# Optimization experiments

Hardware: AMD Instinct MI355X
Metric: run time of the kernel (lower is better)

## Reference

```python
import jax, jax.numpy as jnp
import numpy as np

B, N, H, D = 1, 4096, 16, 64
C = H * D  # 1024
SCALE = D ** -0.5


def setup_inputs() -> dict:
    key = jax.random.key(0)
    k1, k2, k3, k4 = jax.random.split(key, 4)
    x = jax.random.normal(k1, (B, N, C), dtype=jnp.float32)
    # torch nn.Linear weights: [out_features, in_features]; y = x @ W.T + b
    w_qkv = jax.random.normal(k2, (3 * C, C), dtype=jnp.float32) * 0.02
    w_proj = jax.random.normal(k3, (C, C), dtype=jnp.float32) * 0.02
    b_proj = jax.random.normal(k4, (C,), dtype=jnp.float32) * 0.02
    return {"x": x, "w_qkv": w_qkv, "w_proj": w_proj, "b_proj": b_proj}


def reference(x, w_qkv, w_proj, b_proj):
    Bn, Nn, Cn = x.shape
    # fused QKV projection (no bias)
    qkv = jnp.einsum('bnc,oc->bno', x, w_qkv)            # [B,N,3C]
    qkv = qkv.reshape(Bn, Nn, 3, H, D)
    q = jnp.transpose(qkv[:, :, 0], (0, 2, 1, 3))        # [B,H,N,D]
    k = jnp.transpose(qkv[:, :, 1], (0, 2, 1, 3))
    v = jnp.transpose(qkv[:, :, 2], (0, 2, 1, 3))
    attn = jnp.einsum('bhnd,bhmd->bhnm', q, k) * SCALE   # [B,H,N,N]
    causal_mask = jnp.triu(jnp.ones((Nn, Nn), dtype=bool), k=1)
    attn = jnp.where(causal_mask, -jnp.inf, attn)
    attn = jax.nn.softmax(attn, axis=-1)
    out = jnp.einsum('bhnm,bhmd->bhnd', attn, v)          # [B,H,N,D]
    out = jnp.transpose(out, (0, 2, 1, 3)).reshape(Bn, Nn, Cn)
    out = jnp.einsum('bnc,oc->bno', out, w_proj) + b_proj
    return out
```

## Files before the change

### kernel.cpp

```cpp
#include <hip/hip_runtime.h>
#include <hip/hip_bf16.h>
#include <stdint.h>
#include <stddef.h>

using bf16 = __hip_bfloat16;
typedef short short8 __attribute__((ext_vector_type(8)));
typedef short short4v __attribute__((ext_vector_type(4)));
typedef short short2v __attribute__((ext_vector_type(2)));
typedef float f32x4 __attribute__((ext_vector_type(4)));

#define MFMA16(A, B, C) __builtin_amdgcn_mfma_f32_16x16x32_bf16(A, B, C, 0, 0, 0)
#define MFMA16K16(A, B, C) __builtin_amdgcn_mfma_f32_16x16x16bf16_1k(A, B, C, 0, 0, 0)
#define GLOAD_LDS(g, l) __builtin_amdgcn_global_load_lds( \
    (const __attribute__((address_space(1))) void*)(g),   \
    (__attribute__((address_space(3))) void*)(l), 16, 0, 0)

constexpr int AN  = 4096;
constexpr int NH  = 16;
constexpr int HD  = 64;
constexpr int CC  = 1024;
constexpr int C3  = 3072;
constexpr float QSCALE = 0.125f * 1.4426950408889634f;

__device__ inline short bf16s(float f) {
    bf16 h = __float2bfloat16(f);
    return *reinterpret_cast<short*>(&h);
}
__device__ inline float bf2f(short s) {
    return __uint_as_float(((unsigned)(unsigned short)s) << 16);
}
__device__ inline short4v pack4(float a, float b, float c, float d) {
    union { short4v s4; __hip_bfloat162 h2[2]; } u;
    u.h2[0] = __float22bfloat162_rn(make_float2(a, b));
    u.h2[1] = __float22bfloat162_rn(make_float2(c, d));
    return u.s4;
}

__global__ void detect_mode(const unsigned short* __restrict__ xraw,
                            int* __restrict__ mode) {
    const int lane = threadIdx.x;
    int crazy = 0;
    #pragma unroll
    for (int i = 0; i < 4; ++i) {
        const unsigned short u = xraw[lane * 4 + i];
        const int e = (u >> 7) & 0xFF;
        if (e >= 134 || (e != 0 && e <= 110)) ++crazy;
    }
    #pragma unroll
    for (int off = 32; off > 0; off >>= 1)
        crazy += __shfl_down(crazy, off, 64);
    if (lane == 0) *mode = (crazy >= 8) ? 1 : 0;
}

__global__ void cast_in(const void* __restrict__ src, bf16* __restrict__ dst,
                        int n, const int* __restrict__ mode) {
    const int i = (blockIdx.x * blockDim.x + threadIdx.x) * 8;
    if (i >= n) return;
    if (*mode) {
        const float* s = (const float*)src;
        float4 a = *(const float4*)(s + i);
        float4 b = *(const float4*)(s + i + 4);
        short8 o;
        o[0] = bf16s(a.x); o[1] = bf16s(a.y); o[2] = bf16s(a.z); o[3] = bf16s(a.w);
        o[4] = bf16s(b.x); o[5] = bf16s(b.y); o[6] = bf16s(b.z); o[7] = bf16s(b.w);
        *(short8*)(dst + i) = o;
    } else {
        *(short8*)(dst + i) = *(const short8*)((const short*)src + i);
    }
}

__global__ void cast_bias(const void* __restrict__ src, float* __restrict__ dst,
                          int n, const int* __restrict__ mode) {
    const int i = blockIdx.x * blockDim.x + threadIdx.x;
    if (i >= n) return;
    dst[i] = (*mode) ? ((const float*)src)[i]
                     : __bfloat162float(((const bf16*)src)[i]);
}

constexpr int BM = 128, BN = 128, BK = 32;

template<int MODE>
__global__ __launch_bounds__(256, 2) void gemm_bt(
    const bf16* __restrict__ A, const bf16* __restrict__ Bw,
    const float* __restrict__ bias, void* __restrict__ Cout,
    bf16* __restrict__ vTout, const int* __restrict__ mode,
    int M, int K, int O)
{
    __shared__ bf16 As[BM * BK];
    __shared__ bf16 Bs[BN * BK];

    const int tid  = threadIdx.x;
    const int wave = tid >> 6;
    const int lane = tid & 63;
    const int quad = lane >> 4;
    const int l16  = lane & 15;
    const int wr   = wave >> 1;
    const int wc   = wave & 1;
    const int m0   = blockIdx.y * BM;
    const int o0   = blockIdx.x * BN;

    const int srow = lane >> 2;
    const int scol = (lane & 3) * 8;

    f32x4 acc[4][4] = {};

    for (int k0 = 0; k0 < K; k0 += BK) {
        __syncthreads();
        #pragma unroll
        for (int c = 0; c < 2; ++c) {
            const int rbase = wave * 32 + c * 16;
            GLOAD_LDS(A + (size_t)(m0 + rbase + srow) * K + k0 + scol, &As[rbase * BK]);
            GLOAD_LDS(Bw + (size_t)(o0 + rbase + srow) * K + k0 + scol, &Bs[rbase * BK]);
        }
        __syncthreads();

        short8 af[4], bfr[4];
        #pragma unroll
        for (int i = 0; i < 4; ++i)
            af[i] = *(const short8*)&As[(wr * 64 + i * 16 + l16) * BK + quad * 8];
        #pragma unroll
        for (int j = 0; j < 4; ++j)
            bfr[j] = *(const short8*)&Bs[(wc * 64 + j * 16 + l16) * BK + quad * 8];
        #pragma unroll
        for (int i = 0; i < 4; ++i)
            #pragma unroll
            for (int j = 0; j < 4; ++j)
                acc[i][j] = MFMA16(af[i], bfr[j], acc[i][j]);
    }

    if (MODE == 1 && o0 >= 2 * CC) {
        #pragma unroll
        for (int j = 0; j < 4; ++j) {
            const int vc = o0 - 2 * CC + wc * 64 + j * 16 + l16;
            #pragma unroll
            for (int i = 0; i < 4; ++i) {
                const int row0 = m0 + wr * 64 + i * 16 + quad * 4;
                *(short4v*)&vTout[(size_t)vc * AN + row0] =
                    pack4(acc[i][j][0], acc[i][j][1], acc[i][j][2], acc[i][j][3]);
            }
        }
        return;
    }
    const float qs = (MODE == 1 && o0 < CC) ? QSCALE : 1.0f;
    const bool f32out = (MODE == 2) && (*mode != 0);
    #pragma unroll
    for (int j = 0; j < 4; ++j) {
        const int col = o0 + wc * 64 + j * 16 + l16;
        const float bv = bias ? bias[col] : 0.0f;
        #pragma unroll
        for (int i = 0; i < 4; ++i) {
            const int row = m0 + wr * 64 + i * 16 + quad * 4;
            #pragma unroll
            for (int r = 0; r < 4; ++r) {
                const float v = acc[i][j][r] * qs + bv;
                const size_t idx = (size_t)(row + r) * O + col;
                if (f32out) ((float*)Cout)[idx] = v;
                else        ((bf16*)Cout)[idx]  = __float2bfloat16(v);
            }
        }
    }
}

constexpr int TK = 64;

__global__ __launch_bounds__(256, 4) void attn5(
    const bf16* __restrict__ qkv, const bf16* __restrict__ vT,
    bf16* __restrict__ pOn, float* __restrict__ pl)
{
    __shared__ bf16 Ks[2][TK * HD];
    __shared__ bf16 Vs[2][HD * TK];

    const int tid  = threadIdx.x;
    const int wave = tid >> 6;
    const int lane = tid & 63;
    const int quad = lane >> 4;
    const int l16  = lane & 15;
    const int h7   = l16 & 7;
    const int h    = blockIdx.x & 15;
    const int t    = blockIdx.x >> 4;

    short4v ones;
    ones[0] = (short)0x3F80; ones[1] = (short)0x3F80;
    ones[2] = (short)0x3F80; ones[3] = (short)0x3F80;

    const int sr = lane >> 3;
    const int pc = lane & 7;

    #pragma unroll 1
    for (int pp = 0; pp < 2; ++pp) {
        const int tile = pp ? 63 - t : t;
        const int nIt  = tile + 1;
        const int i0   = pp ? ((64 - t) + 1) >> 1 : 0;
        const int i1   = pp ? 64 - t : (t + 2) >> 1;
        const int half = pp;
        const int qw   = tile * 64 + wave * 16;

        short8 qf0, qf1;
        {
            const bf16* qp = qkv + (size_t)(qw + l16) * C3 + h * HD + quad * 8;
            qf0 = *(const short8*)qp;
            qf1 = *(const short8*)(qp + 32);
        }

        f32x4 acc_l = {};
        f32x4 acc_o[4] = {};

        if (i0 < i1) {
            const bf16 *kp[2], *vp[2];
            #pragma unroll
            for (int c = 0; c < 2; ++c) {
                const int row = wave * 16 + c * 8 + sr;
                const int lc  = pc ^ (row & 7);
                kp[c] = qkv + (size_t)(i0 * TK + row) * C3 + CC + h * HD + lc * 8;
                vp[c] = vT + (size_t)(h * HD + row) * AN + i0 * TK + lc * 8;
            }
            auto stage = [&](int p) {
                #pragma unroll
                for (int c = 0; c < 2; ++c) {
                    const int rb = wave * 16 + c * 8;
                    GLOAD_LDS(kp[c], &Ks[p][rb * HD]);
                    GLOAD_LDS(vp[c], &Vs[p][rb * TK]);
                    kp[c] += (size_t)TK * C3;
                    vp[c] += TK;
                }
            };
            stage(0);
            __syncthreads();
            const bool hasdiag = (i1 == nIt);

            for (int it = i0; it < i1; ++it) {
                const int p = (it - i0) & 1;
                if (it + 1 < i1) stage(p ^ 1);

                f32x4 st[4];
                #pragma unroll
                for (int tt = 0; tt < 4; ++tt) {
                    const int row = tt * 16 + l16;
                    short8 kf0 = *(const short8*)&Ks[p][row * HD + ((quad ^ h7) * 8)];
                    short8 kf1 = *(const short8*)&Ks[p][row * HD + (((quad + 4) ^ h7) * 8)];
                    f32x4 a = {};
                    a = MFMA16(kf0, qf0, a);
                    a = MFMA16(kf1, qf1, a);
                    st[tt] = a;
                }

                if (hasdiag && it == i1 - 1) {
                    const int q = qw + l16;
                    const int kv0 = it * TK;
                    #pragma unroll
                    for (int tt = 0; tt < 4; ++tt)
                        #pragma unroll
                        for (int r = 0; r < 4; ++r) {
                            const int kv = kv0 + tt * 16 + quad * 4 + r;
                            st[tt][r] = (kv <= q) ? exp2f(st[tt][r]) : 0.0f;
                        }
                } else {
                    #pragma unroll
                    for (int tt = 0; tt < 4; ++tt)
                        #pragma unroll
                        for (int r = 0; r < 4; ++r)
                            st[tt][r] = exp2f(st[tt][r]);
                }

                #pragma unroll
                for (int tt = 0; tt < 4; ++tt) {
                    const short4v bp = pack4(st[tt][0], st[tt][1], st[tt][2], st[tt][3]);
                    acc_l = MFMA16K16(ones, bp, acc_l);
                    const int pc2 = (2 * tt + (quad >> 1)) ^ h7;
                    #pragma unroll
                    for (int dt = 0; dt < 4; ++dt) {
                        const int row = dt * 16 + l16;
                        short4v vf = *(const short4v*)&Vs[p][row * TK + pc2 * 8 + (quad & 1) * 4];
                        acc_o[dt] = MFMA16K16(vf, bp, acc_o[dt]);
                    }
                }
                __syncthreads();
            }
        }

        const size_t base = (size_t)half * AN * CC + (size_t)(qw + l16) * CC + h * HD;
        #pragma unroll
        for (int dt = 0; dt < 4; ++dt) {
            const int d0 = dt * 16 + quad * 4;
            *(short4v*)&pOn[base + d0] =
                pack4(acc_o[dt][0], acc_o[dt][1], acc_o[dt][2], acc_o[dt][3]);
        }
        if (quad == 0)
            pl[(size_t)half * NH * AN + (size_t)h * AN + qw + l16] = acc_l[0];
    }
}

__global__ __launch_bounds__(128) void combine_halves(
    const bf16* __restrict__ pOn, const float* __restrict__ pl,
    bf16* __restrict__ outp)
{
    const int q  = blockIdx.x;
    const int c0 = threadIdx.x * 8;
    const int h  = c0 >> 6;
    const float l0 = pl[(size_t)h * AN + q];
    const float l1 = pl[(size_t)NH * AN + (size_t)h * AN + q];
    const float L = l0 + l1;
    const float invL = (L > 0.f) ? 1.f / L : 0.f;
    const size_t off = (size_t)q * CC + c0;
    short8 o0 = *(const short8*)&pOn[off];
    short8 o1 = *(const short8*)&pOn[(size_t)AN * CC + off];
    short8 o;
    #pragma unroll
    for (int e = 0; e < 8; e += 2) {
        float v0 = (bf2f(o0[e])     + bf2f(o1[e]))     * invL;
        float v1 = (bf2f(o0[e + 1]) + bf2f(o1[e + 1])) * invL;
        union { short2v s2; __hip_bfloat162 h2; } u;
        u.h2 = __float22bfloat162_rn(make_float2(v0, v1));
        o[e] = u.s2[0]; o[e + 1] = u.s2[1];
    }
    *(short8*)&outp[off] = o;
}

extern "C" void kernel_launch(void* const* d_in, const int* in_sizes, int n_in,
                              void* d_out, int out_size, void* d_ws, size_t ws_size,
                              hipStream_t stream) {
    char* ws = (char*)d_ws;
    bf16*   qkv      = (bf16*)(ws);
    bf16*   attn_out = (bf16*)(ws + 25165824);
    bf16*   vT       = (bf16*)(ws + 33554432);
    bf16*   xb       = (bf16*)(ws + 41943040);
    bf16*   wqkvb    = (bf16*)(ws + 50331648);
    bf16*   wprojb   = (bf16*)(ws + 56623104);
    float*  biasf    = (float*)(ws + 58720256);
    int*    mode     = (int*)(ws + 58724352);
    bf16*   pOn      = (bf16*)(ws + 58728448);
    float*  pl       = (float*)(ws + 75505664);

    detect_mode<<<1, 64, 0, stream>>>((const unsigned short*)d_in[0], mode);
    cast_in<<<(AN * CC) / 8 / 256, 256, 0, stream>>>(d_in[0], xb, AN * CC, mode);
    cast_in<<<(C3 * CC) / 8 / 256, 256, 0, stream>>>(d_in[1], wqkvb, C3 * CC, mode);
    cast_in<<<(CC * CC) / 8 / 256, 256, 0, stream>>>(d_in[2], wprojb, CC * CC, mode);
    cast_bias<<<CC / 256, 256, 0, stream>>>(d_in[3], biasf, CC, mode);

    gemm_bt<1><<<dim3(C3 / BN, AN / BM), 256, 0, stream>>>(
        xb, wqkvb, nullptr, qkv, vT, mode, AN, CC, C3);
    attn5<<<dim3(64 * NH), 256, 0, stream>>>(qkv, vT, pOn, pl);
    combine_halves<<<dim3(AN), 128, 0, stream>>>(pOn, pl, attn_out);
    gemm_bt<2><<<dim3(CC / BN, AN / BM), 256, 0, stream>>>(
        attn_out, wprojb, biasf, d_out, nullptr, mode, AN, CC, CC);
}
```

Baseline: 222.6 us.

## Merge cast kernels, specialize QKV GEMM, use narrower tiles for projection GEMM

Merges the four input cast launches into one cast_all kernel that branches on block index, which removes launch overhead. The generic templated GEMM is split into a QKV-specialized kernel with compile-time K/O and launch bounds raised to 3 blocks per CU. It is also split into a projection kernel with 128x64 tiles, which doubles the block count for the 1024-wide output (256 to 512 blocks) so the CUs stay better occupied. The cost is lower per-block data reuse in the projection GEMM and possible register pressure from the higher occupancy target.

After: 212.2 us. 1.05x faster.

```diff
diff --git a/kernel.cpp b/kernel.cpp
--- a/kernel.cpp
+++ b/kernel.cpp
@@ -52,11 +52,9 @@
     if (lane == 0) *mode = (crazy >= 8) ? 1 : 0;
 }
 
-__global__ void cast_in(const void* __restrict__ src, bf16* __restrict__ dst,
-                        int n, const int* __restrict__ mode) {
-    const int i = (blockIdx.x * blockDim.x + threadIdx.x) * 8;
-    if (i >= n) return;
-    if (*mode) {
+__device__ inline void cast8(const void* __restrict__ src,
+                             bf16* __restrict__ dst, int i, int m) {
+    if (m) {
         const float* s = (const float*)src;
         float4 a = *(const float4*)(s + i);
         float4 b = *(const float4*)(s + i + 4);
@@ -69,22 +67,32 @@
     }
 }
 
-__global__ void cast_bias(const void* __restrict__ src, float* __restrict__ dst,
-                          int n, const int* __restrict__ mode) {
-    const int i = blockIdx.x * blockDim.x + threadIdx.x;
-    if (i >= n) return;
-    dst[i] = (*mode) ? ((const float*)src)[i]
-                     : __bfloat162float(((const bf16*)src)[i]);
+__global__ void cast_all(const void* __restrict__ x, const void* __restrict__ wq,
+                         const void* __restrict__ wp, const void* __restrict__ bp,
+                         bf16* __restrict__ xb, bf16* __restrict__ wqb,
+                         bf16* __restrict__ wpb, float* __restrict__ biasf,
+                         const int* __restrict__ mode) {
+    const int b = blockIdx.x;
+    const int tid = threadIdx.x;
+    const int m = *mode;
+    if (b < 2048) {
+        cast8(x, xb, (b * 256 + tid) * 8, m);
+    } else if (b < 3584) {
+        cast8(wq, wqb, ((b - 2048) * 256 + tid) * 8, m);
+    } else if (b < 4096) {
+        cast8(wp, wpb, ((b - 3584) * 256 + tid) * 8, m);
+    } else {
+        #pragma unroll
+        for (int i = tid; i < CC; i += 256)
+            biasf[i] = m ? ((const float*)bp)[i] : bf2f(((const short*)bp)[i]);
+    }
 }
 
 constexpr int BM = 128, BN = 128, BK = 32;
 
-template<int MODE>
-__global__ __launch_bounds__(256, 2) void gemm_bt(
+__global__ __launch_bounds__(256, 3) void gemm_qkv(
     const bf16* __restrict__ A, const bf16* __restrict__ Bw,
-    const float* __restrict__ bias, void* __restrict__ Cout,
-    bf16* __restrict__ vTout, const int* __restrict__ mode,
-    int M, int K, int O)
+    bf16* __restrict__ Cout, bf16* __restrict__ vTout)
 {
     __shared__ bf16 As[BM * BK];
     __shared__ bf16 Bs[BN * BK];
@@ -104,13 +112,13 @@
 
     f32x4 acc[4][4] = {};
 
-    for (int k0 = 0; k0 < K; k0 += BK) {
+    for (int k0 = 0; k0 < CC; k0 += BK) {
         __syncthreads();
         #pragma unroll
         for (int c = 0; c < 2; ++c) {
             const int rbase = wave * 32 + c * 16;
-            GLOAD_LDS(A + (size_t)(m0 + rbase + srow) * K + k0 + scol, &As[rbase * BK]);
-            GLOAD_LDS(Bw + (size_t)(o0 + rbase + srow) * K + k0 + scol, &Bs[rbase * BK]);
+            GLOAD_LDS(A + (size_t)(m0 + rbase + srow) * CC + k0 + scol, &As[rbase * BK]);
+            GLOAD_LDS(Bw + (size_t)(o0 + rbase + srow) * CC + k0 + scol, &Bs[rbase * BK]);
         }
         __syncthreads();
 
@@ -128,7 +136,7 @@
                 acc[i][j] = MFMA16(af[i], bfr[j], acc[i][j]);
     }
 
-    if (MODE == 1 && o0 >= 2 * CC) {
+    if (o0 >= 2 * CC) {
         #pragma unroll
         for (int j = 0; j < 4; ++j) {
             const int vc = o0 - 2 * CC + wc * 64 + j * 16 + l16;
@@ -141,19 +149,84 @@
         }
         return;
     }
-    const float qs = (MODE == 1 && o0 < CC) ? QSCALE : 1.0f;
-    const bool f32out = (MODE == 2) && (*mode != 0);
+    const float qs = (o0 < CC) ? QSCALE : 1.0f;
     #pragma unroll
     for (int j = 0; j < 4; ++j) {
         const int col = o0 + wc * 64 + j * 16 + l16;
-        const float bv = bias ? bias[col] : 0.0f;
         #pragma unroll
         for (int i = 0; i < 4; ++i) {
             const int row = m0 + wr * 64 + i * 16 + quad * 4;
             #pragma unroll
+            for (int r = 0; r < 4; ++r)
+                Cout[(size_t)(row + r) * C3 + col] = __float2bfloat16(acc[i][j][r] * qs);
+        }
+    }
+}
+
+constexpr int PM = 128, PN = 64, PK = 32;
+
+__global__ __launch_bounds__(256, 2) void gemm_proj(
+    const bf16* __restrict__ A, const bf16* __restrict__ Bw,
+    const float* __restrict__ bias, void* __restrict__ Cout,
+    const int* __restrict__ mode)
+{
+    __shared__ bf16 As[PM * PK];
+    __shared__ bf16 Bs[PN * PK];
+
+    const int tid  = threadIdx.x;
+    const int wave = tid >> 6;
+    const int lane = tid & 63;
+    const int quad = lane >> 4;
+    const int l16  = lane & 15;
+    const int wr   = wave >> 1;
+    const int wc   = wave & 1;
+    const int m0   = blockIdx.y * PM;
+    const int o0   = blockIdx.x * PN;
+    const bool f32out = (*mode != 0);
+
+    const int srow = lane >> 2;
+    const int scol = (lane & 3) * 8;
+
+    f32x4 acc[4][2] = {};
+
+    for (int k0 = 0; k0 < CC; k0 += PK) {
+        __syncthreads();
+        #pragma unroll
+        for (int c = 0; c < 2; ++c) {
+            const int rbase = wave * 32 + c * 16;
+            GLOAD_LDS(A + (size_t)(m0 + rbase + srow) * CC + k0 + scol, &As[rbase * PK]);
+        }
+        {
+            const int rbase = wave * 16;
+            GLOAD_LDS(Bw + (size_t)(o0 + rbase + srow) * CC + k0 + scol, &Bs[rbase * PK]);
+        }
+        __syncthreads();
+
+        short8 af[4], bfr[2];
+        #pragma unroll
+        for (int i = 0; i < 4; ++i)
+            af[i] = *(const short8*)&As[(wr * 64 + i * 16 + l16) * PK + quad * 8];
+        #pragma unroll
+        for (int j = 0; j < 2; ++j)
+            bfr[j] = *(const short8*)&Bs[(wc * 32 + j * 16 + l16) * PK + quad * 8];
+        #pragma unroll
+        for (int i = 0; i < 4; ++i)
+            #pragma unroll
+            for (int j = 0; j < 2; ++j)
+                acc[i][j] = MFMA16(af[i], bfr[j], acc[i][j]);
+    }
+
+    #pragma unroll
+    for (int j = 0; j < 2; ++j) {
+        const int col = o0 + wc * 32 + j * 16 + l16;
+        const float bv = bias[col];
+        #pragma unroll
+        for (int i = 0; i < 4; ++i) {
+            const int row = m0 + wr * 64 + i * 16 + quad * 4;
+            #pragma unroll
             for (int r = 0; r < 4; ++r) {
-                const float v = acc[i][j][r] * qs + bv;
-                const size_t idx = (size_t)(row + r) * O + col;
+                const float v = acc[i][j][r] + bv;
+                const size_t idx = (size_t)(row + r) * CC + col;
                 if (f32out) ((float*)Cout)[idx] = v;
                 else        ((bf16*)Cout)[idx]  = __float2bfloat16(v);
             }
@@ -332,15 +405,12 @@
     float*  pl       = (float*)(ws + 75505664);
 
     detect_mode<<<1, 64, 0, stream>>>((const unsigned short*)d_in[0], mode);
-    cast_in<<<(AN * CC) / 8 / 256, 256, 0, stream>>>(d_in[0], xb, AN * CC, mode);
-    cast_in<<<(C3 * CC) / 8 / 256, 256, 0, stream>>>(d_in[1], wqkvb, C3 * CC, mode);
-    cast_in<<<(CC * CC) / 8 / 256, 256, 0, stream>>>(d_in[2], wprojb, CC * CC, mode);
-    cast_bias<<<CC / 256, 256, 0, stream>>>(d_in[3], biasf, CC, mode);
-
-    gemm_bt<1><<<dim3(C3 / BN, AN / BM), 256, 0, stream>>>(
-        xb, wqkvb, nullptr, qkv, vT, mode, AN, CC, C3);
+    cast_all<<<dim3(4097), 256, 0, stream>>>(
+        d_in[0], d_in[1], d_in[2], d_in[3], xb, wqkvb, wprojb, biasf, mode);
+
+    gemm_qkv<<<dim3(C3 / BN, AN / BM), 256, 0, stream>>>(xb, wqkvb, qkv, vT);
     attn5<<<dim3(64 * NH), 256, 0, stream>>>(qkv, vT, pOn, pl);
     combine_halves<<<dim3(AN), 128, 0, stream>>>(pOn, pl, attn_out);
-    gemm_bt<2><<<dim3(CC / BN, AN / BM), 256, 0, stream>>>(
-        attn_out, wprojb, biasf, d_out, nullptr, mode, AN, CC, CC);
-}
+    gemm_proj<<<dim3(CC / PN, AN / PM), 256, 0, stream>>>(
+        attn_out, wprojb, biasf, d_out, mode);
+}
```
